# Kernel tuning notes

Measured on AMD Instinct MI355X. Metric: run time of the kernel, lower is better.

The kernel has to match this reference:

```python
import jax, jax.numpy as jnp
import numpy as np

N = 100_000          # nodes
E = 1_600_000        # directed edges (avg degree 16)
H = 128              # hidden_dim
OUT = 5              # output_dim (actions)
FOV = 11             # input_dim -> image side
LIN_IN = (FOV - 2) ** 2 * 3  # 243
LN_EPS = 1e-5


def _conv2d(x, w, b):
    # x: [N,3,h,w], w: [3,3,3,3] OIHW, VALID, stride 1
    y = jax.lax.conv_general_dilated(
        x, w, window_strides=(1, 1), padding='VALID',
        dimension_numbers=('NCHW', 'OIHW', 'NCHW'))
    return y + b[None, :, None, None]


def setup_inputs() -> dict:
    key = jax.random.key(0)
    ks = jax.random.split(key, 32)
    r = lambda i, shape, s=0.05: (jax.random.normal(ks[i], shape, jnp.float32) * s)
    inp = {
        'x': jax.random.normal(ks[0], (N, 3, FOV, FOV), jnp.float32),
        'edge_index': jax.random.randint(ks[1], (2, E), 0, N, jnp.int64)
                      if jax.config.jax_enable_x64 else
                      jax.random.randint(ks[1], (2, E), 0, N, jnp.int32),
        # CustomConv params
        'conv_w': r(2, (3, 3, 3, 3)), 'conv_b': r(3, (3,)),
        'conv_self_w': r(4, (3, 3, 3, 3)), 'conv_self_b': r(5, (3,)),
        'lin_w': r(6, (LIN_IN, H)), 'lin_b': r(7, (H,)),
        'lin_self_w': r(8, (LIN_IN, H)), 'lin_self_b': r(9, (H,)),
        # 3 SAGEConv layers: lin_l (aggregated, with bias), lin_r (root, no bias)
        'sage_lw': r(10, (3, H, H)), 'sage_lb': r(11, (3, H)),
        'sage_rw': r(12, (3, H, H)),
        # LayerNorms applied after layers 0,1,2
        'ln_g': jnp.ones((3, H), jnp.float32), 'ln_b': jnp.zeros((3, H), jnp.float32),
        # post_mp MLP (dropout is identity in eval)
        'mlp_w1': r(13, (H, H)), 'mlp_b1': r(14, (H,)),
        'mlp_w2': r(15, (H, OUT)), 'mlp_b2': r(16, (OUT,)),
    }
    return inp


def _layernorm(h, g, b):
    mu = jnp.mean(h, axis=-1, keepdims=True)
    var = jnp.var(h, axis=-1, keepdims=True)
    return (h - mu) * jax.lax.rsqrt(var + LN_EPS) * g + b


def reference(x, edge_index, conv_w, conv_b, conv_self_w, conv_self_b,
              lin_w, lin_b, lin_self_w, lin_self_b,
              sage_lw, sage_lb, sage_rw, ln_g, ln_b,
              mlp_w1, mlp_b1, mlp_w2, mlp_b2):
    src, dst = edge_index[0], edge_index[1]
    valid = (src != dst)  # remove_self_loops (CustomConv only)

    # ---- layer 0: CustomConv (add aggregation) ----
    self_x = jax.nn.relu(_conv2d(x, conv_self_w, conv_self_b).reshape(N, -1))
    self_x = self_x @ lin_self_w + lin_self_b              # [N,H]
    xn = jax.nn.relu(_conv2d(x, conv_w, conv_b).reshape(N, -1))
    xn = xn @ lin_w + lin_b                                # [N,H]
    msgs = xn[src] * valid[:, None].astype(xn.dtype)       # gather + mask self loops
    h = self_x + jax.ops.segment_sum(msgs, dst, num_segments=N)

    # SAGE mean-degree counts (all edges; SAGE does not remove self loops)
    cnt = jnp.maximum(
        jax.ops.segment_sum(jnp.ones((E,), h.dtype), dst, num_segments=N), 1.0)

    emb = h
    for i in range(4):
        if i > 0:
            j = i - 1
            agg = jax.ops.segment_sum(h[src], dst, num_segments=N) / cnt[:, None]
            h = agg @ sage_lw[j] + sage_lb[j] + h @ sage_rw[j]
        emb = h
        h = jax.nn.relu(h)            # dropout p=0.25 is identity in eval
        if i != 3:
            h = _layernorm(h, ln_g[i], ln_b[i])

    # task == 'node': no pooling
    logits = (h @ mlp_w1 + mlp_b1) @ mlp_w2 + mlp_b2
    return emb, jax.nn.log_softmax(logits, axis=1)
```

## Files before the change

### kernel.cpp

```cpp
#include <hip/hip_runtime.h>
#include <hip/hip_bf16.h>

typedef __hip_bfloat16 bf16;
typedef __attribute__((ext_vector_type(8))) short v8s;
typedef __attribute__((ext_vector_type(4))) float v4f;

#define N_NODES 100000
#define N_EDGES 1600000
#define LN_EPS 1e-5f

#define OFF_CONV_W      0
#define OFF_CONV_B      81
#define OFF_CONV_SW     84
#define OFF_CONV_SB     165
#define OFF_LIN_W       168
#define OFF_LIN_B       31272
#define OFF_LIN_SW      31400
#define OFF_LIN_SB      62504
#define OFF_SAGE_LW     62632
#define OFF_SAGE_LB     111784
#define OFF_SAGE_RW     112168
#define OFF_LN_G        161320
#define OFF_LN_B        161704
#define OFF_MLP_W1      162088
#define OFF_MLP_B1      178472
#define OFF_MLP_W2      178600
#define OFF_MLP_B2      179240
#define PARAM_TOTAL     179245

#define WTL_N 65536
#define WTS_N 98304
#define WTM_N 16384

#define CONV_NB 14

__device__ __forceinline__ unsigned short f2b(float f) {
    bf16 h = __float2bfloat16(f);
    return __builtin_bit_cast(unsigned short, h);
}
__device__ __forceinline__ float blo(unsigned u) { return __uint_as_float(u << 16); }
__device__ __forceinline__ float bhi(unsigned u) { return __uint_as_float(u & 0xffff0000u); }
__device__ __forceinline__ unsigned pack2(float lo, float hi) {
    return (unsigned)f2b(lo) | ((unsigned)f2b(hi) << 16);
}

struct Ptr17 { const void* p[17]; };

__global__ void detect_kernel(const unsigned short* __restrict__ xw,
                              const unsigned int* __restrict__ ew,
                              int* __restrict__ flags) {
    __shared__ int sawBigExp, sawHigh;
    if (threadIdx.x == 0) { sawBigExp = 0; sawHigh = 0; }
    __syncthreads();
    int localBig = 0, localHigh = 0;
    for (int i = threadIdx.x; i < 65536; i += 256) {
        unsigned e = (xw[i] >> 7) & 0xFF;
        if (e >= 0xF0) localBig = 1;
    }
    for (int i = threadIdx.x; i < 8192; i += 256) {
        if (ew[2 * i + 1] != 0) localHigh = 1;
    }
    if (localBig) atomicOr(&sawBigExp, 1);
    if (localHigh) atomicOr(&sawHigh, 1);
    __syncthreads();
    if (threadIdx.x == 0) { flags[0] = sawBigExp; flags[1] = sawHigh ? 0 : 1; }
}

__global__ void cvt_params_kernel(Ptr17 ptrs, const int* __restrict__ flags,
                                  float* __restrict__ dst) {
    int i = blockIdx.x * 256 + threadIdx.x;
    if (i >= PARAM_TOTAL) return;
    const int ksz[17] = {81,3,81,3,31104,128,31104,128,49152,384,49152,384,384,16384,128,640,5};
    int seg = 0, off = i;
    while (off >= ksz[seg]) { off -= ksz[seg]; ++seg; }
    float v;
    if (flags[0]) v = ((const float*)ptrs.p[seg])[off];
    else          v = __bfloat162float(((const bf16*)ptrs.p[seg])[off]);
    dst[i] = v;
}

__global__ void cvt2_kernel(const float* __restrict__ P,
                            unsigned short* __restrict__ wtl,
                            unsigned short* __restrict__ wts,
                            unsigned short* __restrict__ wtm) {
    int i = blockIdx.x * 256 + threadIdx.x;
    if (i < WTL_N) {
        int f = i >> 8, k = i & 255;
        float v = 0.f;
        if (k < 243) v = (f < 128) ? P[OFF_LIN_W + k * 128 + f]
                                   : P[OFF_LIN_SW + k * 128 + (f - 128)];
        wtl[i] = f2b(v);
    } else if (i < WTL_N + WTS_N) {
        int j = i - WTL_N; int l = j >> 15; int r = j & 32767; int f = r >> 8; int k = r & 255;
        float v = (k < 128) ? P[OFF_SAGE_LW + l * 16384 + k * 128 + f]
                            : P[OFF_SAGE_RW + l * 16384 + (k - 128) * 128 + f];
        wts[j] = f2b(v);
    } else if (i < WTL_N + WTS_N + WTM_N) {
        int j = i - WTL_N - WTS_N; int f = j >> 7, k = j & 127;
        wtm[j] = f2b(P[OFF_MLP_W1 + k * 128 + f]);
    }
}

__global__ __launch_bounds__(256) void conv_lin_kernel(
    const void* __restrict__ x, const float* __restrict__ P,
    const unsigned short* __restrict__ wtl, const int* __restrict__ flags,
    unsigned short* __restrict__ xnb, float* __restrict__ selfh)
{
    __shared__ float xs[CONV_NB][368];
    __shared__ unsigned short ysb[16][2][256];
    __shared__ float wconv[2][81];
    __shared__ float bconv[2][3];
    int tid = threadIdx.x;
    int n0 = blockIdx.x * CONV_NB;

    if (tid < 81) { wconv[0][tid] = P[OFF_CONV_W + tid]; wconv[1][tid] = P[OFF_CONV_SW + tid]; }
    else if (tid < 84) { int o = tid - 81; bconv[0][o] = P[OFF_CONV_B + o]; bconv[1][o] = P[OFF_CONV_SB + o]; }

    {
        unsigned int* z = (unsigned int*)ysb;
        #pragma unroll
        for (int i = tid; i < 16 * 2 * 128; i += 256) z[i] = 0;
    }
    if (flags[0]) {
        const float* xf = (const float*)x;
        for (int i = tid; i < CONV_NB * 363; i += 256) {
            int j = i / 363, q = i - j * 363;
            int node = n0 + j;
            xs[j][q] = (node < N_NODES) ? xf[(size_t)node * 363 + q] : 0.f;
        }
    } else {
        const unsigned short* xb = (const unsigned short*)x;
        for (int i = tid; i < CONV_NB * 363; i += 256) {
            int j = i / 363, q = i - j * 363;
            int node = n0 + j;
            xs[j][q] = (node < N_NODES) ? blo(xb[(size_t)node * 363 + q]) : 0.f;
        }
    }
    __syncthreads();

    if (tid < CONV_NB * 18) {
        int j = tid / 18, rem = tid - j * 18;
        int p = rem / 9, oi = rem - p * 9;
        float acc[27];
        #pragma unroll
        for (int o = 0; o < 3; o++) {
            float b = bconv[p][o];
            #pragma unroll
            for (int oj = 0; oj < 9; oj++) acc[o * 9 + oj] = b;
        }
        #pragma unroll
        for (int c = 0; c < 3; c++) {
            #pragma unroll
            for (int ki = 0; ki < 3; ki++) {
                float xr[11];
                const float* row = &xs[j][c * 121 + (oi + ki) * 11];
                #pragma unroll
                for (int t = 0; t < 11; t++) xr[t] = row[t];
                #pragma unroll
                for (int o = 0; o < 3; o++) {
                    int wb = o * 27 + c * 9 + ki * 3;
                    float w0 = wconv[p][wb], w1 = wconv[p][wb + 1], w2 = wconv[p][wb + 2];
                    #pragma unroll
                    for (int oj = 0; oj < 9; oj++)
                        acc[o * 9 + oj] += xr[oj] * w0 + xr[oj + 1] * w1 + xr[oj + 2] * w2;
                }
            }
        }
        #pragma unroll
        for (int o = 0; o < 3; o++)
            #pragma unroll
            for (int oj = 0; oj < 9; oj++)
                ysb[j][p][o * 81 + oi * 9 + oj] = f2b(fmaxf(acc[o * 9 + oj], 0.f));
    }
    __syncthreads();

    int wave = tid >> 6, lane = tid & 63, quad = lane >> 4, col = lane & 15;
    int p = wave >> 1;
    v4f acc[4];
    #pragma unroll
    for (int t = 0; t < 4; t++) { acc[t][0] = 0.f; acc[t][1] = 0.f; acc[t][2] = 0.f; acc[t][3] = 0.f; }
    for (int s = 0; s < 8; s++) {
        int kq = s * 32 + quad * 8;
        v8s a = *(const v8s*)&ysb[col][p][kq];
        #pragma unroll
        for (int t = 0; t < 4; t++) {
            int f = (wave * 4 + t) * 16 + col;
            v8s b = *(const v8s*)&wtl[(size_t)f * 256 + kq];
            acc[t] = __builtin_amdgcn_mfma_f32_16x16x32_bf16(a, b, acc[t], 0, 0, 0);
        }
    }
    #pragma unroll
    for (int t = 0; t < 4; t++) {
        int f = (wave * 4 + t) * 16 + col;
        #pragma unroll
        for (int r = 0; r < 4; r++) {
            int jj = quad * 4 + r;
            int node = n0 + jj;
            if (jj < CONV_NB && node < N_NODES) {
                float v = acc[t][r];
                if (p == 0) xnb[(size_t)node * 128 + f] = f2b(v + P[OFF_LIN_B + f]);
                else        selfh[(size_t)node * 128 + (f - 128)] = v + P[OFF_LIN_SB + (f - 128)];
            }
        }
    }
}

__device__ __forceinline__ int ld_edge(const int* __restrict__ ew, size_t elem, int isi64) {
    size_t idx = isi64 ? (elem * 2) : elem;
    return ew[idx];
}

__global__ void degree_kernel(const int* __restrict__ ew, const int* __restrict__ flags,
                              int* __restrict__ deg) {
    int e = blockIdx.x * blockDim.x + threadIdx.x;
    if (e < N_EDGES) {
        int d = ld_edge(ew, (size_t)N_EDGES + e, flags[1]);
        if ((unsigned)d < N_NODES) atomicAdd(&deg[d], 1);
    }
}

__global__ __launch_bounds__(1024) void scanA(const int* __restrict__ deg, int* __restrict__ rowptr,
                                              float* __restrict__ cntf, int* __restrict__ bsum) {
    __shared__ int s[1024];
    int tid = threadIdx.x;
    int i = blockIdx.x * 1024 + tid;
    int v = (i < N_NODES) ? deg[i] : 0;
    s[tid] = v;
    __syncthreads();
    for (int off = 1; off < 1024; off <<= 1) {
        int t = (tid >= off) ? s[tid - off] : 0;
        __syncthreads();
        s[tid] += t;
        __syncthreads();
    }
    if (i < N_NODES) {
        rowptr[i] = s[tid] - v;
        cntf[i] = (float)(v < 1 ? 1 : v);
    }
    if (tid == 1023) bsum[blockIdx.x] = s[1023];
}

__global__ void scanB(const int* __restrict__ bsum, int* __restrict__ boff, int nb, int* __restrict__ rowptr_end) {
    if (threadIdx.x == 0 && blockIdx.x == 0) {
        int run = 0;
        for (int i = 0; i < nb; i++) { boff[i] = run; run += bsum[i]; }
        *rowptr_end = run;
    }
}

__global__ __launch_bounds__(1024) void scanC(int* __restrict__ rowptr, const int* __restrict__ boff,
                                              int* __restrict__ cursor) {
    int i = blockIdx.x * 1024 + threadIdx.x;
    if (i < N_NODES) {
        int v = rowptr[i] + boff[blockIdx.x];
        rowptr[i] = v;
        cursor[i] = v;
    }
}

__global__ void fill_kernel(const int* __restrict__ ew, const int* __restrict__ flags,
                            int* __restrict__ cursor, int* __restrict__ csr) {
    int e = blockIdx.x * blockDim.x + threadIdx.x;
    if (e < N_EDGES) {
        int isi64 = flags[1];
        int s = ld_edge(ew, (size_t)e, isi64);
        int d = ld_edge(ew, (size_t)N_EDGES + e, isi64);
        if ((unsigned)d < N_NODES) {
            int p = atomicAdd(&cursor[d], 1);
            if ((unsigned)p < N_EDGES)
                csr[p] = ((unsigned)s < N_NODES) ? (s | ((s == d) ? (int)0x80000000 : 0)) : -1;
        }
    }
}

__global__ __launch_bounds__(256) void agg0ln_kernel(const unsigned short* __restrict__ xnb,
        const float* __restrict__ selfh, const int* __restrict__ rowptr, const int* __restrict__ csr,
        const float* __restrict__ lng, const float* __restrict__ lnb,
        unsigned short* __restrict__ zb) {
    int wave = threadIdx.x >> 6, lane = threadIdx.x & 63;
    int g = lane >> 4, c = lane & 15;
    int n = blockIdx.x * 4 + wave;
    int beg = rowptr[n], end = rowptr[n + 1];
    float a[8];
    #pragma unroll
    for (int i = 0; i < 8; i++) a[i] = 0.f;
    const uint4* x4 = (const uint4*)xnb;
    for (int b = beg; b < end; b += 64) {
        int bl = b + lane;
        int my = (bl < end) ? csr[bl] : -1;
        int nb = end - b; if (nb > 64) nb = 64;
        for (int i = 0; i < nb; i += 8) {
            int sv0 = __shfl(my, i + g, 64);
            int sv1 = __shfl(my, i + 4 + g, 64);
            bool va0 = ((unsigned)sv0 < N_NODES);
            bool va1 = ((unsigned)sv1 < N_NODES);
            uint4 v0 = x4[(size_t)(va0 ? sv0 : 0) * 16 + c];
            uint4 v1 = x4[(size_t)(va1 ? sv1 : 0) * 16 + c];
            if (va0) {
                a[0] += blo(v0.x); a[1] += bhi(v0.x);
                a[2] += blo(v0.y); a[3] += bhi(v0.y);
                a[4] += blo(v0.z); a[5] += bhi(v0.z);
                a[6] += blo(v0.w); a[7] += bhi(v0.w);
            }
            if (va1) {
                a[0] += blo(v1.x); a[1] += bhi(v1.x);
                a[2] += blo(v1.y); a[3] += bhi(v1.y);
                a[4] += blo(v1.z); a[5] += bhi(v1.z);
                a[6] += blo(v1.w); a[7] += bhi(v1.w);
            }
        }
    }
    #pragma unroll
    for (int i = 0; i < 8; i++) {
        a[i] += __shfl_xor(a[i], 16, 64);
        a[i] += __shfl_xor(a[i], 32, 64);
    }
    if (g == 0) {
        const float4* s4 = (const float4*)(selfh + (size_t)n * 128 + c * 8);
        float4 s0 = s4[0], s1 = s4[1];
        float v[8];
        v[0] = s0.x + a[0]; v[1] = s0.y + a[1]; v[2] = s0.z + a[2]; v[3] = s0.w + a[3];
        v[4] = s1.x + a[4]; v[5] = s1.y + a[5]; v[6] = s1.z + a[6]; v[7] = s1.w + a[7];
        float s = 0.f, sq = 0.f;
        #pragma unroll
        for (int i = 0; i < 8; i++) {
            v[i] = fmaxf(v[i], 0.f);
            s += v[i]; sq += v[i] * v[i];
        }
        #pragma unroll
        for (int m = 8; m >= 1; m >>= 1) {
            s  += __shfl_xor(s, m, 64);
            sq += __shfl_xor(sq, m, 64);
        }
        float mu = s * (1.f / 128.f);
        float var = sq * (1.f / 128.f) - mu * mu;
        float is = rsqrtf(var + LN_EPS);
        const float4* g4 = (const float4*)(lng + c * 8);
        const float4* b4 = (const float4*)(lnb + c * 8);
        float4 g0 = g4[0], g1 = g4[1], b0 = b4[0], b1 = b4[1];
        float z[8];
        z[0] = (v[0] - mu) * is * g0.x + b0.x; z[1] = (v[1] - mu) * is * g0.y + b0.y;
        z[2] = (v[2] - mu) * is * g0.z + b0.z; z[3] = (v[3] - mu) * is * g0.w + b0.w;
        z[4] = (v[4] - mu) * is * g1.x + b1.x; z[5] = (v[5] - mu) * is * g1.y + b1.y;
        z[6] = (v[6] - mu) * is * g1.z + b1.z; z[7] = (v[7] - mu) * is * g1.w + b1.w;
        uint4 o;
        o.x = pack2(z[0], z[1]); o.y = pack2(z[2], z[3]);
        o.z = pack2(z[4], z[5]); o.w = pack2(z[6], z[7]);
        ((uint4*)zb)[(size_t)n * 16 + c] = o;
    }
}

__global__ __launch_bounds__(256) void aggm_kernel(const unsigned short* __restrict__ zb,
        const int* __restrict__ rowptr, const int* __restrict__ csr,
        const float* __restrict__ cntf, unsigned short* __restrict__ aggb) {
    int wave = threadIdx.x >> 6, lane = threadIdx.x & 63;
    int g = lane >> 4, c = lane & 15;
    int n = blockIdx.x * 4 + wave;
    int beg = rowptr[n], end = rowptr[n + 1];
    float a[8];
    #pragma unroll
    for (int i = 0; i < 8; i++) a[i] = 0.f;
    const uint4* z4 = (const uint4*)zb;
    for (int b = beg; b < end; b += 64) {
        int bl = b + lane;
        int my = (bl < end) ? csr[bl] : -1;
        int nb = end - b; if (nb > 64) nb = 64;
        for (int i = 0; i < nb; i += 8) {
            int sv0 = __shfl(my, i + g, 64) & 0x7fffffff;
            int sv1 = __shfl(my, i + 4 + g, 64) & 0x7fffffff;
            bool va0 = (sv0 < N_NODES);
            bool va1 = (sv1 < N_NODES);
            uint4 v0 = z4[(size_t)(va0 ? sv0 : 0) * 16 + c];
            uint4 v1 = z4[(size_t)(va1 ? sv1 : 0) * 16 + c];
            if (va0) {
                a[0] += blo(v0.x); a[1] += bhi(v0.x);
                a[2] += blo(v0.y); a[3] += bhi(v0.y);
                a[4] += blo(v0.z); a[5] += bhi(v0.z);
                a[6] += blo(v0.w); a[7] += bhi(v0.w);
            }
            if (va1) {
                a[0] += blo(v1.x); a[1] += bhi(v1.x);
                a[2] += blo(v1.y); a[3] += bhi(v1.y);
                a[4] += blo(v1.z); a[5] += bhi(v1.z);
                a[6] += blo(v1.w); a[7] += bhi(v1.w);
            }
        }
    }
    #pragma unroll
    for (int i = 0; i < 8; i++) {
        a[i] += __shfl_xor(a[i], 16, 64);
        a[i] += __shfl_xor(a[i], 32, 64);
    }
    if (g == 0) {
        float inv = 1.f / cntf[n];
        uint4 o;
        o.x = pack2(a[0] * inv, a[1] * inv); o.y = pack2(a[2] * inv, a[3] * inv);
        o.z = pack2(a[4] * inv, a[5] * inv); o.w = pack2(a[6] * inv, a[7] * inv);
        ((uint4*)aggb)[(size_t)n * 16 + c] = o;
    }
}

__global__ __launch_bounds__(256) void sageln_kernel(const unsigned short* __restrict__ aggb,
        unsigned short* __restrict__ zb, const unsigned short* __restrict__ wts,
        const float* __restrict__ lb, const float* __restrict__ lng, const float* __restrict__ lnb,
        int last, float* __restrict__ hout) {
    __shared__ float hb[16][128];
    int tid = threadIdx.x;
    int n0 = blockIdx.x * 16;
    int wave = tid >> 6, lane = tid & 63, quad = lane >> 4, col = lane & 15;
    int nodeA = n0 + col;

    v4f acc[2];
    #pragma unroll
    for (int t = 0; t < 2; t++) { acc[t][0] = 0.f; acc[t][1] = 0.f; acc[t][2] = 0.f; acc[t][3] = 0.f; }
    #pragma unroll
    for (int s = 0; s < 8; s++) {
        int kq = s * 32 + quad * 8;
        const unsigned short* abase = (s < 4) ? (aggb + (size_t)nodeA * 128 + kq)
                                              : (zb + (size_t)nodeA * 128 + (kq - 128));
        v8s a = *(const v8s*)abase;
        #pragma unroll
        for (int t = 0; t < 2; t++) {
            int f = (wave * 2 + t) * 16 + col;
            v8s b = *(const v8s*)&wts[(size_t)f * 256 + kq];
            acc[t] = __builtin_amdgcn_mfma_f32_16x16x32_bf16(a, b, acc[t], 0, 0, 0);
        }
    }
    #pragma unroll
    for (int t = 0; t < 2; t++) {
        int f = (wave * 2 + t) * 16 + col;
        float bias = lb[f];
        #pragma unroll
        for (int r = 0; r < 4; r++)
            hb[quad * 4 + r][f] = acc[t][r] + bias;
    }
    __syncthreads();

    #pragma unroll
    for (int jj = 0; jj < 4; jj++) {
        int j = wave * 4 + jj;
        int node = n0 + j;
        float v0 = hb[j][2 * lane], v1 = hb[j][2 * lane + 1];
        if (last) {
            float2 w; w.x = v0; w.y = v1;
            ((float2*)hout)[(size_t)node * 64 + lane] = w;
        } else {
            float r0 = fmaxf(v0, 0.f), r1 = fmaxf(v1, 0.f);
            float s = r0 + r1, sq = r0 * r0 + r1 * r1;
            #pragma unroll
            for (int m = 32; m >= 1; m >>= 1) {
                s  += __shfl_xor(s, m, 64);
                sq += __shfl_xor(sq, m, 64);
            }
            float mu = s * (1.f / 128.f);
            float var = sq * (1.f / 128.f) - mu * mu;
            float inv = rsqrtf(var + LN_EPS);
            float z0 = (r0 - mu) * inv * lng[2 * lane]     + lnb[2 * lane];
            float z1 = (r1 - mu) * inv * lng[2 * lane + 1] + lnb[2 * lane + 1];
            ((unsigned int*)zb)[(size_t)node * 64 + lane] = pack2(z0, z1);
        }
    }
}

__global__ __launch_bounds__(256) void mlp_kernel(const float* __restrict__ h,
        const unsigned short* __restrict__ wtm, const float* __restrict__ P,
        const int* __restrict__ flags, void* __restrict__ out) {
    __shared__ unsigned short rb[16][128];
    __shared__ float mb[16][128];
    __shared__ float lg[16][5];
    int tid = threadIdx.x;
    int n0 = blockIdx.x * 16;
    int isf = flags[0];

    const float2* h2 = (const float2*)h;
    for (int i = tid; i < 16 * 64; i += 256) {
        int j = i >> 6, q = i & 63;
        float2 v = h2[(size_t)(n0 + j) * 64 + q];
        size_t oi = (size_t)(n0 + j) * 128 + 2 * q;
        if (isf) { ((float*)out)[oi] = v.x; ((float*)out)[oi + 1] = v.y; }
        else ((unsigned int*)out)[oi >> 1] = pack2(v.x, v.y);
        rb[j][2 * q]     = f2b(fmaxf(v.x, 0.f));
        rb[j][2 * q + 1] = f2b(fmaxf(v.y, 0.f));
    }
    __syncthreads();

    int wave = tid >> 6, lane = tid & 63, quad = lane >> 4, col = lane & 15;
    v4f acc[2];
    #pragma unroll
    for (int t = 0; t < 2; t++) { acc[t][0] = 0.f; acc[t][1] = 0.f; acc[t][2] = 0.f; acc[t][3] = 0.f; }
    #pragma unroll
    for (int s = 0; s < 4; s++) {
        int kq = s * 32 + quad * 8;
        v8s a = *(const v8s*)&rb[col][kq];
        #pragma unroll
        for (int t = 0; t < 2; t++) {
            int f = (wave * 2 + t) * 16 + col;
            v8s b = *(const v8s*)&wtm[(size_t)f * 128 + kq];
            acc[t] = __builtin_amdgcn_mfma_f32_16x16x32_bf16(a, b, acc[t], 0, 0, 0);
        }
    }
    #pragma unroll
    for (int t = 0; t < 2; t++) {
        int f = (wave * 2 + t) * 16 + col;
        float bias = P[OFF_MLP_B1 + f];
        #pragma unroll
        for (int r = 0; r < 4; r++)
            mb[quad * 4 + r][f] = acc[t][r] + bias;
    }
    __syncthreads();

    if (tid < 80) {
        int j = tid / 5, o = tid - (tid / 5) * 5;
        float a = P[OFF_MLP_B2 + o];
        for (int k = 0; k < 128; k++) a += mb[j][k] * P[OFF_MLP_W2 + k * 5 + o];
        lg[j][o] = a;
    }
    __syncthreads();
    if (tid < 16) {
        int j = tid;
        float mx = lg[j][0];
        #pragma unroll
        for (int o = 1; o < 5; o++) mx = fmaxf(mx, lg[j][o]);
        float se = 0.f;
        #pragma unroll
        for (int o = 0; o < 5; o++) se += expf(lg[j][o] - mx);
        float lse = mx + logf(se);
        size_t base = (size_t)N_NODES * 128 + (size_t)(n0 + j) * 5;
        #pragma unroll
        for (int o = 0; o < 5; o++) {
            float v = lg[j][o] - lse;
            if (isf) ((float*)out)[base + o] = v;
            else     ((bf16*)out)[base + o] = __float2bfloat16(v);
        }
    }
}

extern "C" void kernel_launch(void* const* d_in, const int* in_sizes, int n_in,
                              void* d_out, int out_size, void* d_ws, size_t ws_size,
                              hipStream_t stream) {
    const void* x  = d_in[0];
    const int*  ew = (const int*)d_in[1];

    Ptr17 ptrs;
    for (int i = 0; i < 17; i++) ptrs.p[i] = d_in[2 + i];

    char* w = (char*)d_ws;
    auto carve = [&](size_t bytes) { char* r = w; w += (bytes + 255) & ~(size_t)255; return r; };
    float*          bufS  = (float*)carve((size_t)N_NODES * 128 * 4);
    unsigned short* xnb   = (unsigned short*)carve((size_t)N_NODES * 128 * 2);
    unsigned short* zb    = (unsigned short*)carve((size_t)N_NODES * 128 * 2);
    unsigned short* aggb  = (unsigned short*)carve((size_t)N_NODES * 128 * 2);
    float*          pf32  = (float*)carve((size_t)PARAM_TOTAL * 4);
    unsigned short* wtl   = (unsigned short*)carve((size_t)WTL_N * 2);
    unsigned short* wts   = (unsigned short*)carve((size_t)WTS_N * 2);
    unsigned short* wtm   = (unsigned short*)carve((size_t)WTM_N * 2);
    int*   deg    = (int*)carve((size_t)N_NODES * 4);
    int*   rowptr = (int*)carve((size_t)(N_NODES + 64) * 4);
    int*   cursor = (int*)carve((size_t)N_NODES * 4);
    float* cntf   = (float*)carve((size_t)N_NODES * 4);
    int*   bsum   = (int*)carve(512);
    int*   boff   = (int*)carve(512);
    int*   flags  = (int*)carve(256);
    int*   csr    = (int*)carve((size_t)N_EDGES * 4);

    const int SCAN_BLOCKS = (N_NODES + 1023) / 1024;
    const int CONV_BLOCKS = (N_NODES + CONV_NB - 1) / CONV_NB;

    detect_kernel<<<1, 256, 0, stream>>>((const unsigned short*)x, (const unsigned int*)ew, flags);
    cvt_params_kernel<<<(PARAM_TOTAL + 255) / 256, 256, 0, stream>>>(ptrs, flags, pf32);
    cvt2_kernel<<<(WTL_N + WTS_N + WTM_N + 255) / 256, 256, 0, stream>>>(pf32, wtl, wts, wtm);

    hipMemsetAsync(deg, 0, (size_t)N_NODES * 4, stream);

    conv_lin_kernel<<<CONV_BLOCKS, 256, 0, stream>>>(x, pf32, wtl, flags, xnb, bufS);

    degree_kernel<<<(N_EDGES + 255) / 256, 256, 0, stream>>>(ew, flags, deg);
    scanA<<<SCAN_BLOCKS, 1024, 0, stream>>>(deg, rowptr, cntf, bsum);
    scanB<<<1, 1, 0, stream>>>(bsum, boff, SCAN_BLOCKS, rowptr + N_NODES);
    scanC<<<SCAN_BLOCKS, 1024, 0, stream>>>(rowptr, boff, cursor);
    fill_kernel<<<(N_EDGES + 255) / 256, 256, 0, stream>>>(ew, flags, cursor, csr);

    agg0ln_kernel<<<N_NODES / 4, 256, 0, stream>>>(xnb, bufS, rowptr, csr,
        pf32 + OFF_LN_G, pf32 + OFF_LN_B, zb);

    for (int l = 0; l < 3; l++) {
        aggm_kernel<<<N_NODES / 4, 256, 0, stream>>>(zb, rowptr, csr, cntf, aggb);
        sageln_kernel<<<N_NODES / 16, 256, 0, stream>>>(aggb, zb, wts + (size_t)l * 32768,
            pf32 + OFF_SAGE_LB + l * 128,
            pf32 + OFF_LN_G + (l + 1) * 128, pf32 + OFF_LN_B + (l + 1) * 128,
            (l == 2) ? 1 : 0, bufS);
    }

    mlp_kernel<<<N_NODES / 16, 256, 0, stream>>>(bufS, wtm, pf32, flags, d_out);
}
```

Measured before the change: 1.217 ms.

## Split fused conv+linear kernel into separate conv and MFMA linear kernels

Replaces the fused conv_lin kernel with a conv-only kernel that writes padded bf16 ReLU activations (two 100k×256 buffers) to global memory, followed by two MFMA-based linear kernels that read them back. This is meant to raise occupancy and parallelism in each stage, since the fused kernel's shared-memory and register use capped throughput. The cost is about 100 MB of extra global write and read traffic plus extra launches. The split runs only when the workspace is large enough; otherwise the old fused path is used.

```diff
diff --git a/kernel.cpp b/kernel.cpp
--- a/kernel.cpp
+++ b/kernel.cpp
@@ -33,6 +33,7 @@
 #define WTM_N 16384
 
 #define CONV_NB 14
+#define CONVA_NB 9
 
 __device__ __forceinline__ unsigned short f2b(float f) {
     bf16 h = __float2bfloat16(f);
@@ -101,6 +102,122 @@
     }
 }
 
+__global__ __launch_bounds__(256) void convA_kernel(
+    const void* __restrict__ x, const float* __restrict__ P, const int* __restrict__ flags,
+    unsigned short* __restrict__ yb0, unsigned short* __restrict__ yb1)
+{
+    __shared__ float xs[CONVA_NB][364];
+    __shared__ float wc[2][81];
+    __shared__ float bc[2][3];
+    int tid = threadIdx.x;
+    int n0 = blockIdx.x * CONVA_NB;
+
+    if (tid < 81) { wc[0][tid] = P[OFF_CONV_W + tid]; wc[1][tid] = P[OFF_CONV_SW + tid]; }
+    else if (tid < 84) { int o = tid - 81; bc[0][o] = P[OFF_CONV_B + o]; bc[1][o] = P[OFF_CONV_SB + o]; }
+
+    if (flags[0]) {
+        const float* xf = (const float*)x;
+        #pragma unroll
+        for (int j = 0; j < CONVA_NB; j++) {
+            int node = n0 + j;
+            const float* src = xf + (size_t)node * 363;
+            for (int q = tid; q < 363; q += 256)
+                xs[j][q] = (node < N_NODES) ? src[q] : 0.f;
+        }
+    } else {
+        const unsigned short* xb = (const unsigned short*)x;
+        #pragma unroll
+        for (int j = 0; j < CONVA_NB; j++) {
+            int node = n0 + j;
+            const unsigned short* src = xb + (size_t)node * 363;
+            for (int q = tid; q < 363; q += 256)
+                xs[j][q] = (node < N_NODES) ? blo(src[q]) : 0.f;
+        }
+    }
+    __syncthreads();
+
+    if (tid < CONVA_NB * 27) {
+        int j = tid / 27, rem = tid % 27;
+        int o = rem / 9, oi = rem % 9;
+        int node = n0 + j;
+        float a0[9], a1[9];
+        float b0v = bc[0][o], b1v = bc[1][o];
+        #pragma unroll
+        for (int oj = 0; oj < 9; oj++) { a0[oj] = b0v; a1[oj] = b1v; }
+        #pragma unroll
+        for (int c = 0; c < 3; c++) {
+            #pragma unroll
+            for (int ki = 0; ki < 3; ki++) {
+                float xr[11];
+                const float* row = &xs[j][c * 121 + (oi + ki) * 11];
+                #pragma unroll
+                for (int t = 0; t < 11; t++) xr[t] = row[t];
+                int wb = o * 27 + c * 9 + ki * 3;
+                float w00 = wc[0][wb], w01 = wc[0][wb + 1], w02 = wc[0][wb + 2];
+                float w10 = wc[1][wb], w11 = wc[1][wb + 1], w12 = wc[1][wb + 2];
+                #pragma unroll
+                for (int oj = 0; oj < 9; oj++) {
+                    a0[oj] += xr[oj] * w00 + xr[oj + 1] * w01 + xr[oj + 2] * w02;
+                    a1[oj] += xr[oj] * w10 + xr[oj + 1] * w11 + xr[oj + 2] * w12;
+                }
+            }
+        }
+        if (node < N_NODES) {
+            size_t base = (size_t)node * 256 + o * 81 + oi * 9;
+            #pragma unroll
+            for (int oj = 0; oj < 9; oj++) {
+                yb0[base + oj] = f2b(fmaxf(a0[oj], 0.f));
+                yb1[base + oj] = f2b(fmaxf(a1[oj], 0.f));
+            }
+        }
+    }
+    for (int i = tid; i < CONVA_NB * 13; i += 256) {
+        int j = i / 13, k = 243 + (i - j * 13);
+        int node = n0 + j;
+        if (node < N_NODES) {
+            yb0[(size_t)node * 256 + k] = 0;
+            yb1[(size_t)node * 256 + k] = 0;
+        }
+    }
+}
+
+__global__ __launch_bounds__(256) void linB_kernel(
+    const unsigned short* __restrict__ yb, const unsigned short* __restrict__ wt,
+    const float* __restrict__ bias, int store_bf16,
+    unsigned short* __restrict__ outb, float* __restrict__ outf)
+{
+    int tid = threadIdx.x;
+    int n0 = blockIdx.x * 16;
+    int wave = tid >> 6, lane = tid & 63, quad = lane >> 4, col = lane & 15;
+    int nodeA = n0 + col;
+    v4f acc[2];
+    #pragma unroll
+    for (int t = 0; t < 2; t++) { acc[t][0] = 0.f; acc[t][1] = 0.f; acc[t][2] = 0.f; acc[t][3] = 0.f; }
+    #pragma unroll
+    for (int s = 0; s < 8; s++) {
+        int kq = s * 32 + quad * 8;
+        v8s a = *(const v8s*)&yb[(size_t)nodeA * 256 + kq];
+        #pragma unroll
+        for (int t = 0; t < 2; t++) {
+            int f = (wave * 2 + t) * 16 + col;
+            v8s b = *(const v8s*)&wt[(size_t)f * 256 + kq];
+            acc[t] = __builtin_amdgcn_mfma_f32_16x16x32_bf16(a, b, acc[t], 0, 0, 0);
+        }
+    }
+    #pragma unroll
+    for (int t = 0; t < 2; t++) {
+        int f = (wave * 2 + t) * 16 + col;
+        float bv = bias[f];
+        #pragma unroll
+        for (int r = 0; r < 4; r++) {
+            int node = n0 + quad * 4 + r;
+            float v = acc[t][r] + bv;
+            if (store_bf16) outb[(size_t)node * 128 + f] = f2b(v);
+            else            outf[(size_t)node * 128 + f] = v;
+        }
+    }
+}
+
 __global__ __launch_bounds__(256) void conv_lin_kernel(
     const void* __restrict__ x, const float* __restrict__ P,
     const unsigned short* __restrict__ wtl, const int* __restrict__ flags,
@@ -562,9 +679,11 @@
     int*   boff   = (int*)carve(512);
     int*   flags  = (int*)carve(256);
     int*   csr    = (int*)carve((size_t)N_EDGES * 4);
+    unsigned short* yb0 = (unsigned short*)carve((size_t)N_NODES * 256 * 2);
+    unsigned short* yb1 = (unsigned short*)carve((size_t)N_NODES * 256 * 2);
+    bool use_split = ((size_t)(w - (char*)d_ws) <= ws_size);
 
     const int SCAN_BLOCKS = (N_NODES + 1023) / 1024;
-    const int CONV_BLOCKS = (N_NODES + CONV_NB - 1) / CONV_NB;
 
     detect_kernel<<<1, 256, 0, stream>>>((const unsigned short*)x, (const unsigned int*)ew, flags);
     cvt_params_kernel<<<(PARAM_TOTAL + 255) / 256, 256, 0, stream>>>(ptrs, flags, pf32);
@@ -572,7 +691,15 @@
 
     hipMemsetAsync(deg, 0, (size_t)N_NODES * 4, stream);
 
-    conv_lin_kernel<<<CONV_BLOCKS, 256, 0, stream>>>(x, pf32, wtl, flags, xnb, bufS);
+    if (use_split) {
+        const int CA_BLOCKS = (N_NODES + CONVA_NB - 1) / CONVA_NB;
+        convA_kernel<<<CA_BLOCKS, 256, 0, stream>>>(x, pf32, flags, yb0, yb1);
+        linB_kernel<<<N_NODES / 16, 256, 0, stream>>>(yb0, wtl, pf32 + OFF_LIN_B, 1, xnb, nullptr);
+        linB_kernel<<<N_NODES / 16, 256, 0, stream>>>(yb1, wtl + (size_t)128 * 256, pf32 + OFF_LIN_SB, 0, nullptr, bufS);
+    } else {
+        const int CONV_BLOCKS = (N_NODES + CONV_NB - 1) / CONV_NB;
+        conv_lin_kernel<<<CONV_BLOCKS, 256, 0, stream>>>(x, pf32, wtl, flags, xnb, bufS);
+    }
 
     degree_kernel<<<(N_EDGES + 255) / 256, 256, 0, stream>>>(ew, flags, deg);
     scanA<<<SCAN_BLOCKS, 1024, 0, stream>>>(deg, rowptr, cntf, bsum);
```

Result: slower. 1.383 ms (+13.6%).
